# Performance work log

Measured on AMD Instinct MI355X. Metric: run time of the kernel, lower is better.

## Reference

```python
import jax, jax.numpy as jnp
import numpy as np

N, F_IN, F_OUT, P, E = 50000, 64, 64, 8, 800000


def setup_inputs() -> dict:
    key = jax.random.key(0)
    ks = jax.random.split(key, 11)
    s = 0.05
    X = jax.random.normal(ks[0], (N, F_IN, P), jnp.float32)
    edge_index = jax.random.randint(ks[1], (2, E), 0, N)
    edge_weight = jax.random.uniform(ks[2], (E,), jnp.float32)
    # Stacked ChebConv (K=2) params for gates [i, f, c, o]
    Wx0 = jax.random.normal(ks[3], (4, F_IN, F_OUT), jnp.float32) * s
    Wx1 = jax.random.normal(ks[4], (4, F_IN, F_OUT), jnp.float32) * s
    bx = jax.random.normal(ks[5], (4, F_OUT), jnp.float32) * s
    Wh0 = jax.random.normal(ks[6], (4, F_OUT, F_OUT), jnp.float32) * s
    Wh1 = jax.random.normal(ks[7], (4, F_OUT, F_OUT), jnp.float32) * s
    bh = jax.random.normal(ks[8], (4, F_OUT), jnp.float32) * s
    wc = jax.random.normal(ks[9], (3, F_OUT), jnp.float32) * s  # peepholes for i, f, o
    bg = jax.random.normal(ks[10], (4, F_OUT), jnp.float32) * s  # gate biases i, f, c, o
    return dict(X=X, edge_index=edge_index, edge_weight=edge_weight,
                Wx0=Wx0, Wx1=Wx1, bx=bx, Wh0=Wh0, Wh1=Wh1, bh=bh, wc=wc, bg=bg)


def reference(X, edge_index, edge_weight, Wx0, Wx1, bx, Wh0, Wh1, bh, wc, bg):
    src, dst = edge_index[0], edge_index[1]
    # sym-normalized Laplacian, scaled by 2/lambda_max with lambda_max=2, minus I:
    # L_hat = -D^{-1/2} A D^{-1/2}  (diagonal cancels exactly in ChebConv.__norm__)
    deg = jax.ops.segment_sum(edge_weight, src, num_segments=N)
    dis = jnp.where(deg > 0, jax.lax.rsqrt(jnp.maximum(deg, 1e-12)), 0.0)
    wn = -dis[src] * edge_weight * dis[dst]  # [E]

    def cheb(x, W0, W1, b):
        # ChebConv K=2: T0(x)=x, T1(x)=L_hat x ; out = x@W0 + (L_hat x)@W1 + b
        tx1 = jax.ops.segment_sum(wn[:, None] * x[src], dst, num_segments=N)
        return x @ W0 + tx1 @ W1 + b

    def step(Xp):  # one GConvLSTM step from zero hidden/cell state (H=None, C=None)
        H = jnp.zeros((N, F_OUT), X.dtype)
        C = jnp.zeros((N, F_OUT), X.dtype)
        I = jax.nn.sigmoid(cheb(Xp, Wx0[0], Wx1[0], bx[0]) + cheb(H, Wh0[0], Wh1[0], bh[0]) + wc[0] * C + bg[0])
        Fg = jax.nn.sigmoid(cheb(Xp, Wx0[1], Wx1[1], bx[1]) + cheb(H, Wh0[1], Wh1[1], bh[1]) + wc[1] * C + bg[1])
        T = jnp.tanh(cheb(Xp, Wx0[2], Wx1[2], bx[2]) + cheb(H, Wh0[2], Wh1[2], bh[2]) + bg[2])
        Cn = Fg * C + I * T
        O = jax.nn.sigmoid(cheb(Xp, Wx0[3], Wx1[3], bx[3]) + cheb(H, Wh0[3], Wh1[3], bh[3]) + wc[2] * Cn + bg[3])
        return O * jnp.tanh(Cn)

    # periods are independent (fresh zero state each period) -> vmap then sum
    Hs = jax.vmap(step)(jnp.moveaxis(X, 2, 0))  # [P, N, F_OUT]
    return Hs.sum(axis=0)
```

## Files before the change

kernel.cpp:

```cpp
#include <hip/hip_runtime.h>
#include <hip/hip_fp16.h>

#define NN 50000
#define EE 800000
#define FF 64
#define PP 8
#define NPAD 50048
#define ELLW 64
#define NB_BUILD 1024
#define NB_XPOSE 12500
#define NB_WPACK 96

typedef _Float16 half8 __attribute__((ext_vector_type(8)));
typedef _Float16 half4 __attribute__((ext_vector_type(4)));
typedef float floatx4 __attribute__((ext_vector_type(4)));

static constexpr size_t al512(size_t x) { return (x + 511) & ~size_t(511); }
static constexpr size_t OFF_DEG  = 0;
static constexpr size_t OFF_CNT  = al512(OFF_DEG  + (size_t)NN*4);
static constexpr size_t OFF_END0 = al512(OFF_CNT  + (size_t)NN*4);
static constexpr size_t OFF_ELL  = OFF_END0;
static constexpr size_t OFF_BIAS = al512(OFF_ELL  + (size_t)NN*ELLW*8);
static constexpr size_t OFF_WC2  = al512(OFF_BIAS + 192*4);
static constexpr size_t OFF_WFRG = al512(OFF_WC2  + 64*4);
static constexpr size_t OFF_XB   = al512(OFF_WFRG + (size_t)24576*2);
static constexpr size_t OFF_TB   = al512(OFF_XB   + (size_t)NPAD*512*2);

__global__ void k_bx(const int* __restrict__ src, const int* __restrict__ dst,
                     const float* __restrict__ ew,
                     float* __restrict__ deg, int* __restrict__ cnt,
                     int2* __restrict__ ell,
                     const float* __restrict__ X, _Float16* __restrict__ XB,
                     const float* __restrict__ Wx0, const float* __restrict__ Wx1,
                     const float* __restrict__ bx, const float* __restrict__ bh,
                     const float* __restrict__ wc, const float* __restrict__ bg,
                     _Float16* __restrict__ Wfrag, float* __restrict__ biasv,
                     float* __restrict__ wc2) {
    __shared__ _Float16 tile[4][512];
    int b = blockIdx.x;
    if (b < NB_BUILD) {
        const int stride = NB_BUILD * 256;
#pragma unroll 2
        for (int e = b * 256 + threadIdx.x; e < EE; e += stride) {
            int s = src[e], d = dst[e];
            float w = ew[e];
            atomicAdd(deg + s, w);
            int pos = atomicAdd(cnt + d, 1);
            if (pos < ELLW) {
                int2 pr; pr.x = s; pr.y = __float_as_int(w);
                ell[(size_t)d * ELLW + pos] = pr;
            }
        }
    } else if (b < NB_BUILD + NB_XPOSE) {
        int wid = threadIdx.x >> 6, lane = threadIdx.x & 63;
        int n = (b - NB_BUILD) * 4 + wid;
        const float4* xp = (const float4*)(X + (size_t)n * 512 + lane * 8);
        float4 a = xp[0], c = xp[1];
        float v[8] = {a.x, a.y, a.z, a.w, c.x, c.y, c.z, c.w};
#pragma unroll
        for (int p = 0; p < PP; ++p)
            tile[wid][p * 64 + lane] = (_Float16)v[p];
        half8 vv = *(const half8*)&tile[wid][lane * 8];
        *(half8*)(XB + (size_t)n * 512 + lane * 8) = vv;
    } else if (b < NB_BUILD + NB_XPOSE + NB_WPACK) {
        const int gmap[3] = {0, 2, 3};
        int t = (b - NB_BUILD - NB_XPOSE) * 256 + threadIdx.x;
        int j8 = t & 7;
        int lane = (t >> 3) & 63;
        int rem = t >> 9;
        int ct = rem % 12;
        int ks = rem / 12;
        int k = ks * 32 + (lane >> 4) * 8 + j8;
        int gp = ct >> 2;
        int g = gmap[gp];
        int j64 = (ct & 3) * 16 + (lane & 15);
        float val = (k < 64) ? Wx0[((size_t)g * 64 + k) * 64 + j64]
                             : Wx1[((size_t)g * 64 + (k - 64)) * 64 + j64];
        Wfrag[t] = (_Float16)val;
    } else {
        const int gmap[3] = {0, 2, 3};
        int t = threadIdx.x;
        if (t < 192) {
            int gp = t / 64, j = t % 64;
            int g = gmap[gp];
            biasv[t] = bx[g * 64 + j] + bh[g * 64 + j] + bg[g * 64 + j];
        } else {
            int j = t - 192;
            wc2[j] = wc[2 * 64 + j];
        }
    }
}

__global__ void k_spmm(const _Float16* __restrict__ XB, const int* __restrict__ cnt,
                       const float* __restrict__ deg, const int2* __restrict__ ell,
                       _Float16* __restrict__ TB) {
    int wid = threadIdx.x >> 6, lane = threadIdx.x & 63;
    int b = blockIdx.x;
    int half = b & 1;
    int n = (b >> 1) * 4 + wid;
    if (n >= NN) return;
    float acc[4] = {0.f, 0.f, 0.f, 0.f};
    int cn = min(cnt[n], ELLW);
    float dgn = deg[n];
    float dn = dgn > 0.f ? rsqrtf(fmaxf(dgn, 1e-12f)) : 0.f;
    const int foff = half * 256 + lane * 4;
    if (cn > 0) {
        const int2* __restrict__ row = ell + (size_t)n * ELLW;
        int2 ed = row[min(lane, cn - 1)];
        float dgs = deg[ed.x];
        float dsr = dgs > 0.f ? rsqrtf(fmaxf(dgs, 1e-12f)) : 0.f;
        float wl = (lane < cn) ? dsr * __int_as_float(ed.y) : 0.f;
        int wli = __float_as_int(wl);
        for (int base = 0; base < cn; base += 16) {
            half4 r[16];
            float wk[16];
#pragma unroll
            for (int u = 0; u < 16; ++u) {
                int srck = __builtin_amdgcn_readlane(ed.x, base + u);
                wk[u] = __int_as_float(__builtin_amdgcn_readlane(wli, base + u));
                r[u] = *(const half4*)(XB + (size_t)srck * 512 + foff);
            }
#pragma unroll
            for (int u = 0; u < 16; ++u) {
#pragma unroll
                for (int j = 0; j < 4; ++j) acc[j] += wk[u] * (float)r[u][j];
            }
        }
    }
    half4 st;
#pragma unroll
    for (int j = 0; j < 4; ++j) st[j] = (_Float16)(-dn * acc[j]);
    *(half4*)(TB + (size_t)n * 512 + foff) = st;
}

__device__ __forceinline__ float fast_rcp(float x) { return __builtin_amdgcn_rcpf(x); }
__device__ __forceinline__ float sigmoidf_fast(float x) {
    return fast_rcp(1.f + __expf(-x));
}
__device__ __forceinline__ float tanhf_fast(float x) {
    return 1.f - 2.f * fast_rcp(1.f + __expf(2.f * x));
}

__global__ __launch_bounds__(128) void k_gemm(const _Float16* __restrict__ XB,
                                              const _Float16* __restrict__ TB,
                                              const _Float16* __restrict__ Wfrag,
                                              const float* __restrict__ biasv,
                                              const float* __restrict__ wc2,
                                              float* __restrict__ out) {
    const int tid = threadIdx.x;
    const int w = tid >> 6;
    const int lane = tid & 63;
    const half8* __restrict__ Wg8 = (const half8*)Wfrag;

    const int n0 = blockIdx.x * 32;
    const int jj = lane & 15, quad = lane >> 4;

    half8 Bf[2][3][4];
#pragma unroll
    for (int c4l = 0; c4l < 2; ++c4l)
#pragma unroll
        for (int gp = 0; gp < 3; ++gp)
#pragma unroll
            for (int ks = 0; ks < 4; ++ks)
                Bf[c4l][gp][ks] = Wg8[(ks * 12 + gp * 4 + (w * 2 + c4l)) * 64 + lane];

    float bi[2], bc[2], bo[2], wcv[2];
#pragma unroll
    for (int c4l = 0; c4l < 2; ++c4l) {
        int j = (w * 2 + c4l) * 16 + jj;
        bi[c4l] = biasv[j];
        bc[c4l] = biasv[64 + j];
        bo[c4l] = biasv[128 + j];
        wcv[c4l] = wc2[j];
    }

    const _Float16* __restrict__ x0 = XB + (size_t)(n0 + jj) * 512;
    const _Float16* __restrict__ x1 = XB + (size_t)(n0 + 16 + jj) * 512;
    const _Float16* __restrict__ t0 = TB + (size_t)(n0 + jj) * 512;
    const _Float16* __restrict__ t1 = TB + (size_t)(n0 + 16 + jj) * 512;

    floatx4 outacc[2][2];
#pragma unroll
    for (int r = 0; r < 2; ++r)
#pragma unroll
        for (int c4l = 0; c4l < 2; ++c4l) outacc[r][c4l] = (floatx4){0.f, 0.f, 0.f, 0.f};

#pragma unroll 1
    for (int p = 0; p < PP; ++p) {
        const int o = p * 64 + quad * 8;
        half8 a00 = *(const half8*)(x0 + o);
        half8 a01 = *(const half8*)(x0 + o + 32);
        half8 a02 = *(const half8*)(t0 + o);
        half8 a03 = *(const half8*)(t0 + o + 32);
        half8 a10 = *(const half8*)(x1 + o);
        half8 a11 = *(const half8*)(x1 + o + 32);
        half8 a12 = *(const half8*)(t1 + o);
        half8 a13 = *(const half8*)(t1 + o + 32);
#pragma unroll
        for (int c4l = 0; c4l < 2; ++c4l) {
            floatx4 ai0 = {0.f,0.f,0.f,0.f}, ac0 = {0.f,0.f,0.f,0.f}, ao0 = {0.f,0.f,0.f,0.f};
            floatx4 ai1 = {0.f,0.f,0.f,0.f}, ac1 = {0.f,0.f,0.f,0.f}, ao1 = {0.f,0.f,0.f,0.f};
#pragma unroll
            for (int ks = 0; ks < 4; ++ks) {
                half8 a0 = (ks == 0) ? a00 : (ks == 1) ? a01 : (ks == 2) ? a02 : a03;
                half8 a1 = (ks == 0) ? a10 : (ks == 1) ? a11 : (ks == 2) ? a12 : a13;
                ai0 = __builtin_amdgcn_mfma_f32_16x16x32_f16(a0, Bf[c4l][0][ks], ai0, 0, 0, 0);
                ai1 = __builtin_amdgcn_mfma_f32_16x16x32_f16(a1, Bf[c4l][0][ks], ai1, 0, 0, 0);
                ac0 = __builtin_amdgcn_mfma_f32_16x16x32_f16(a0, Bf[c4l][1][ks], ac0, 0, 0, 0);
                ac1 = __builtin_amdgcn_mfma_f32_16x16x32_f16(a1, Bf[c4l][1][ks], ac1, 0, 0, 0);
                ao0 = __builtin_amdgcn_mfma_f32_16x16x32_f16(a0, Bf[c4l][2][ks], ao0, 0, 0, 0);
                ao1 = __builtin_amdgcn_mfma_f32_16x16x32_f16(a1, Bf[c4l][2][ks], ao1, 0, 0, 0);
            }
#pragma unroll
            for (int rr = 0; rr < 4; ++rr) {
                float I0 = sigmoidf_fast(ai0[rr] + bi[c4l]);
                float T0 = tanhf_fast(ac0[rr] + bc[c4l]);
                float Cn0 = I0 * T0;
                float O0 = sigmoidf_fast(ao0[rr] + bo[c4l] + wcv[c4l] * Cn0);
                outacc[0][c4l][rr] += O0 * tanhf_fast(Cn0);
                float I1 = sigmoidf_fast(ai1[rr] + bi[c4l]);
                float T1 = tanhf_fast(ac1[rr] + bc[c4l]);
                float Cn1 = I1 * T1;
                float O1 = sigmoidf_fast(ao1[rr] + bo[c4l] + wcv[c4l] * Cn1);
                outacc[1][c4l][rr] += O1 * tanhf_fast(Cn1);
            }
        }
    }
#pragma unroll
    for (int r = 0; r < 2; ++r)
#pragma unroll
        for (int c4l = 0; c4l < 2; ++c4l)
#pragma unroll
            for (int rr = 0; rr < 4; ++rr) {
                int n = n0 + r * 16 + quad * 4 + rr;
                if (n < NN) out[(size_t)n * 64 + (w * 2 + c4l) * 16 + jj] = outacc[r][c4l][rr];
            }
}

extern "C" void kernel_launch(void* const* d_in, const int* in_sizes, int n_in,
                              void* d_out, int out_size, void* d_ws, size_t ws_size,
                              hipStream_t stream) {
    const float* X   = (const float*)d_in[0];
    const int*   ei  = (const int*)d_in[1];
    const float* ew  = (const float*)d_in[2];
    const float* Wx0 = (const float*)d_in[3];
    const float* Wx1 = (const float*)d_in[4];
    const float* bx  = (const float*)d_in[5];
    const float* bh  = (const float*)d_in[8];
    const float* wc  = (const float*)d_in[9];
    const float* bg  = (const float*)d_in[10];
    float* out = (float*)d_out;

    const int* src = ei;
    const int* dst = ei + EE;

    char* ws = (char*)d_ws;
    float* deg     = (float*)(ws + OFF_DEG);
    int*   cnt     = (int*)(ws + OFF_CNT);
    int2*  ell     = (int2*)(ws + OFF_ELL);
    float* biasv   = (float*)(ws + OFF_BIAS);
    float* wc2     = (float*)(ws + OFF_WC2);
    _Float16* Wfrag = (_Float16*)(ws + OFF_WFRG);
    _Float16* XB    = (_Float16*)(ws + OFF_XB);
    _Float16* TB    = (_Float16*)(ws + OFF_TB);

    hipMemsetAsync(ws, 0, OFF_END0, stream);

    k_bx<<<NB_BUILD + NB_XPOSE + NB_WPACK + 1, 256, 0, stream>>>(
        src, dst, ew, deg, cnt, ell, X, XB,
        Wx0, Wx1, bx, bh, wc, bg, Wfrag, biasv, wc2);
    k_spmm<<<2 * (NN / 4), 256, 0, stream>>>(XB, cnt, deg, ell, TB);
    k_gemm<<<NPAD / 32, 128, 0, stream>>>(XB, TB, Wfrag, biasv, wc2, out);
}
```

Baseline: 414.1 us.

## Fuse SpMM into gate GEMM kernel via swizzled shared-memory T tile

Merges the sparse aggregation kernel into the MFMA gate kernel. Each 128-thread block first gathers neighbour rows for its 32 nodes into a 32x512 fp16 LDS tile with an XOR swizzle, then runs the GEMM reading T from LDS. This removes the global round trip of the TB buffer and one kernel launch. The cost is lower gather parallelism per block: 2 waves each handle 16 rows serially with 8-wide loads, and the 32KB of LDS limits occupancy. The edge-build loop unroll is also reduced to 1.

```diff
diff --git a/kernel.cpp b/kernel.cpp
--- a/kernel.cpp
+++ b/kernel.cpp
@@ -12,7 +12,6 @@
 #define NB_WPACK 96
 
 typedef _Float16 half8 __attribute__((ext_vector_type(8)));
-typedef _Float16 half4 __attribute__((ext_vector_type(4)));
 typedef float floatx4 __attribute__((ext_vector_type(4)));
 
 static constexpr size_t al512(size_t x) { return (x + 511) & ~size_t(511); }
@@ -24,7 +23,6 @@
 static constexpr size_t OFF_WC2  = al512(OFF_BIAS + 192*4);
 static constexpr size_t OFF_WFRG = al512(OFF_WC2  + 64*4);
 static constexpr size_t OFF_XB   = al512(OFF_WFRG + (size_t)24576*2);
-static constexpr size_t OFF_TB   = al512(OFF_XB   + (size_t)NPAD*512*2);
 
 __global__ void k_bx(const int* __restrict__ src, const int* __restrict__ dst,
                      const float* __restrict__ ew,
@@ -40,7 +38,7 @@
     int b = blockIdx.x;
     if (b < NB_BUILD) {
         const int stride = NB_BUILD * 256;
-#pragma unroll 2
+#pragma unroll 1
         for (int e = b * 256 + threadIdx.x; e < EE; e += stride) {
             int s = src[e], d = dst[e];
             float w = ew[e];
@@ -91,48 +89,6 @@
     }
 }
 
-__global__ void k_spmm(const _Float16* __restrict__ XB, const int* __restrict__ cnt,
-                       const float* __restrict__ deg, const int2* __restrict__ ell,
-                       _Float16* __restrict__ TB) {
-    int wid = threadIdx.x >> 6, lane = threadIdx.x & 63;
-    int b = blockIdx.x;
-    int half = b & 1;
-    int n = (b >> 1) * 4 + wid;
-    if (n >= NN) return;
-    float acc[4] = {0.f, 0.f, 0.f, 0.f};
-    int cn = min(cnt[n], ELLW);
-    float dgn = deg[n];
-    float dn = dgn > 0.f ? rsqrtf(fmaxf(dgn, 1e-12f)) : 0.f;
-    const int foff = half * 256 + lane * 4;
-    if (cn > 0) {
-        const int2* __restrict__ row = ell + (size_t)n * ELLW;
-        int2 ed = row[min(lane, cn - 1)];
-        float dgs = deg[ed.x];
-        float dsr = dgs > 0.f ? rsqrtf(fmaxf(dgs, 1e-12f)) : 0.f;
-        float wl = (lane < cn) ? dsr * __int_as_float(ed.y) : 0.f;
-        int wli = __float_as_int(wl);
-        for (int base = 0; base < cn; base += 16) {
-            half4 r[16];
-            float wk[16];
-#pragma unroll
-            for (int u = 0; u < 16; ++u) {
-                int srck = __builtin_amdgcn_readlane(ed.x, base + u);
-                wk[u] = __int_as_float(__builtin_amdgcn_readlane(wli, base + u));
-                r[u] = *(const half4*)(XB + (size_t)srck * 512 + foff);
-            }
-#pragma unroll
-            for (int u = 0; u < 16; ++u) {
-#pragma unroll
-                for (int j = 0; j < 4; ++j) acc[j] += wk[u] * (float)r[u][j];
-            }
-        }
-    }
-    half4 st;
-#pragma unroll
-    for (int j = 0; j < 4; ++j) st[j] = (_Float16)(-dn * acc[j]);
-    *(half4*)(TB + (size_t)n * 512 + foff) = st;
-}
-
 __device__ __forceinline__ float fast_rcp(float x) { return __builtin_amdgcn_rcpf(x); }
 __device__ __forceinline__ float sigmoidf_fast(float x) {
     return fast_rcp(1.f + __expf(-x));
@@ -141,18 +97,62 @@
     return 1.f - 2.f * fast_rcp(1.f + __expf(2.f * x));
 }
 
-__global__ __launch_bounds__(128) void k_gemm(const _Float16* __restrict__ XB,
-                                              const _Float16* __restrict__ TB,
-                                              const _Float16* __restrict__ Wfrag,
-                                              const float* __restrict__ biasv,
-                                              const float* __restrict__ wc2,
-                                              float* __restrict__ out) {
+__global__ __launch_bounds__(128) void k_sg(const _Float16* __restrict__ XB,
+                                            const int* __restrict__ cnt,
+                                            const float* __restrict__ deg,
+                                            const int2* __restrict__ ell,
+                                            const _Float16* __restrict__ Wfrag,
+                                            const float* __restrict__ biasv,
+                                            const float* __restrict__ wc2,
+                                            float* __restrict__ out) {
+    __shared__ _Float16 Tl[32][512];
     const int tid = threadIdx.x;
     const int w = tid >> 6;
     const int lane = tid & 63;
+    const int n0 = blockIdx.x * 32;
+
+#pragma unroll 1
+    for (int r = 0; r < 16; ++r) {
+        const int lr = w * 16 + r;
+        const int n = n0 + lr;
+        float acc[8] = {0.f, 0.f, 0.f, 0.f, 0.f, 0.f, 0.f, 0.f};
+        float dn = 0.f;
+        if (n < NN) {
+            int cn = min(cnt[n], ELLW);
+            float dgn = deg[n];
+            dn = dgn > 0.f ? rsqrtf(fmaxf(dgn, 1e-12f)) : 0.f;
+            if (cn > 0) {
+                const int2* __restrict__ row = ell + (size_t)n * ELLW;
+                int2 ed = row[min(lane, cn - 1)];
+                float dgs = deg[ed.x];
+                float dsr = dgs > 0.f ? rsqrtf(fmaxf(dgs, 1e-12f)) : 0.f;
+                float wl = (lane < cn) ? dsr * __int_as_float(ed.y) : 0.f;
+                int wli = __float_as_int(wl);
+                for (int base = 0; base < cn; base += 16) {
+                    half8 rg[16];
+                    float wk[16];
+#pragma unroll
+                    for (int u = 0; u < 16; ++u) {
+                        int srck = __builtin_amdgcn_readlane(ed.x, base + u);
+                        wk[u] = __int_as_float(__builtin_amdgcn_readlane(wli, base + u));
+                        rg[u] = *((const half8*)(XB + (size_t)srck * 512) + lane);
+                    }
+#pragma unroll
+                    for (int u = 0; u < 16; ++u) {
+#pragma unroll
+                        for (int j = 0; j < 8; ++j) acc[j] += wk[u] * (float)rg[u][j];
+                    }
+                }
+            }
+        }
+        half8 st;
+#pragma unroll
+        for (int j = 0; j < 8; ++j) st[j] = (_Float16)(-dn * acc[j]);
+        ((half8*)&Tl[lr][0])[lane ^ (lr & 7)] = st;
+    }
+    __syncthreads();
+
     const half8* __restrict__ Wg8 = (const half8*)Wfrag;
-
-    const int n0 = blockIdx.x * 32;
     const int jj = lane & 15, quad = lane >> 4;
 
     half8 Bf[2][3][4];
@@ -176,8 +176,7 @@
 
     const _Float16* __restrict__ x0 = XB + (size_t)(n0 + jj) * 512;
     const _Float16* __restrict__ x1 = XB + (size_t)(n0 + 16 + jj) * 512;
-    const _Float16* __restrict__ t0 = TB + (size_t)(n0 + jj) * 512;
-    const _Float16* __restrict__ t1 = TB + (size_t)(n0 + 16 + jj) * 512;
+    const int sw0 = jj & 7;
 
     floatx4 outacc[2][2];
 #pragma unroll
@@ -188,14 +187,15 @@
 #pragma unroll 1
     for (int p = 0; p < PP; ++p) {
         const int o = p * 64 + quad * 8;
+        const int c8 = p * 8 + quad;
         half8 a00 = *(const half8*)(x0 + o);
         half8 a01 = *(const half8*)(x0 + o + 32);
-        half8 a02 = *(const half8*)(t0 + o);
-        half8 a03 = *(const half8*)(t0 + o + 32);
+        half8 a02 = ((const half8*)&Tl[jj][0])[c8 ^ sw0];
+        half8 a03 = ((const half8*)&Tl[jj][0])[(c8 + 4) ^ sw0];
         half8 a10 = *(const half8*)(x1 + o);
         half8 a11 = *(const half8*)(x1 + o + 32);
-        half8 a12 = *(const half8*)(t1 + o);
-        half8 a13 = *(const half8*)(t1 + o + 32);
+        half8 a12 = ((const half8*)&Tl[16 + jj][0])[c8 ^ sw0];
+        half8 a13 = ((const half8*)&Tl[16 + jj][0])[(c8 + 4) ^ sw0];
 #pragma unroll
         for (int c4l = 0; c4l < 2; ++c4l) {
             floatx4 ai0 = {0.f,0.f,0.f,0.f}, ac0 = {0.f,0.f,0.f,0.f}, ao0 = {0.f,0.f,0.f,0.f};
@@ -262,13 +262,11 @@
     float* wc2     = (float*)(ws + OFF_WC2);
     _Float16* Wfrag = (_Float16*)(ws + OFF_WFRG);
     _Float16* XB    = (_Float16*)(ws + OFF_XB);
-    _Float16* TB    = (_Float16*)(ws + OFF_TB);
 
     hipMemsetAsync(ws, 0, OFF_END0, stream);
 
     k_bx<<<NB_BUILD + NB_XPOSE + NB_WPACK + 1, 256, 0, stream>>>(
         src, dst, ew, deg, cnt, ell, X, XB,
         Wx0, Wx1, bx, bh, wc, bg, Wfrag, biasv, wc2);
-    k_spmm<<<2 * (NN / 4), 256, 0, stream>>>(XB, cnt, deg, ell, TB);
-    k_gemm<<<NPAD / 32, 128, 0, stream>>>(XB, TB, Wfrag, biasv, wc2, out);
-}
+    k_sg<<<NPAD / 32, 128, 0, stream>>>(XB, cnt, deg, ell, Wfrag, biasv, wc2, out);
+}
```

Measured after the change: 420.3 us. About the same (+1.5%).
